# Performance work log

Hardware: AMD Instinct MI355X
Metric: run time of the kernel (lower is better)

Reference implementation:

```python
import jax, jax.numpy as jnp
import numpy as np

EPS = 1e-12


def setup_inputs() -> dict:
    key = jax.random.key(0)
    k1, k2, k3, k4 = jax.random.split(key, 4)
    N, H, W, D, K = 64, 32, 32, 512, 64
    x = jax.random.normal(k1, (N, H, W, D), dtype=jnp.float32)
    W_assign = jax.random.normal(k2, (D, K), dtype=jnp.float32) * 0.05  # 1x1 conv kernel
    b_assign = jax.random.normal(k3, (K,), dtype=jnp.float32) * 0.05
    C = jax.random.normal(k4, (D, K), dtype=jnp.float32) * 0.05  # cluster centers
    return {"x": x, "W_assign": W_assign, "b_assign": b_assign, "C": C}


def _l2norm(v, axis):
    return v / jnp.sqrt(jnp.sum(v * v, axis=axis, keepdims=True) + EPS)


def reference(x, W_assign, b_assign, C):
    # 1x1 conv = matmul over channel dim: [N,H,W,D] @ [D,K] -> [N,H,W,K]
    s = jnp.einsum('nhwd,dk->nhwk', x, W_assign) + b_assign
    a = jax.nn.softmax(s, axis=-1)                       # soft assignment over K
    # VLAD: v[n,d,k] = sum_hw a[n,h,w,k] * (x[n,h,w,d] + C[d,k])
    # reformulated as two small contractions (no [N,H,W,D,K] intermediate):
    v = jnp.einsum('nhwd,nhwk->ndk', x, a)               # feature-weighted sums
    a_sum = jnp.sum(a, axis=(1, 2))                      # [N,K]
    v = v + a_sum[:, None, :] * C[None, :, :]            # [N,D,K]
    # intra-normalization: L2 over D per cluster (after transpose to [N,K,D])
    v = _l2norm(jnp.transpose(v, (0, 2, 1)), axis=-1)    # [N,K,D]
    v = jnp.transpose(v, (0, 2, 1))                      # [N,D,K]
    # flatten and final L2 normalize -> [N, D*K]
    v = v.reshape(v.shape[0], -1)
    return _l2norm(v, axis=-1)
```

## Files before the change

kernel.cpp:

```cpp
#include <hip/hip_runtime.h>


#define EPSF 1e-12f

typedef short bf16x8 __attribute__((ext_vector_type(8)));
typedef float f32x16 __attribute__((ext_vector_type(16)));

__device__ inline unsigned short f2bf_rne(float f) {
  union { float f; unsigned u; } v; v.f = f;
  unsigned u = v.u;
  unsigned r = u + 0x7fffu + ((u >> 16) & 1u);
  return (unsigned short)(r >> 16);
}
__device__ inline unsigned pk2(float a, float b) {
  return (unsigned)f2bf_rne(a) | ((unsigned)f2bf_rne(b) << 16);
}

__global__ __launch_bounds__(256) void kprep(
    const float* __restrict__ Wm, unsigned short* __restrict__ wt) {
  __shared__ float tile[64][65];
  const int t = threadIdx.x, bx = blockIdx.x;
  {
    int col = (t & 15) * 4, rbase = t >> 4;
#pragma unroll
    for (int r = 0; r < 4; ++r) {
      int row = rbase + 16 * r;
      *(float4*)&tile[row][col] =
          *(const float4*)&Wm[(size_t)(bx * 64 + row) * 64 + col];
    }
  }
  __syncthreads();
  int k = t >> 2, seg = (t & 3) * 16;
  size_t o = (size_t)k * 512 + bx * 64 + seg;
#pragma unroll
  for (int j = 0; j < 16; j += 2)
    *(unsigned*)&wt[o + j] = pk2(tile[seg + j][k], tile[seg + j + 1][k]);
}

__global__ __launch_bounds__(256) void kconv(
    const float* __restrict__ x, unsigned short* __restrict__ xt) {
  __shared__ unsigned short td[64][66];
  const int t = threadIdx.x;
  const int hw0 = (blockIdx.x & 15) * 64, d0 = (blockIdx.x >> 4) * 64;
  const int n = blockIdx.y;
  {
    int c = (t & 15) * 4, r0 = t >> 4;
#pragma unroll
    for (int rr = 0; rr < 4; ++rr) {
      int row = r0 + 16 * rr;
      float4 v = *(const float4*)&x[((size_t)(n * 1024 + hw0 + row)) * 512 + d0 + c];
      *(unsigned*)&td[row][c] = pk2(v.x, v.y);
      *(unsigned*)&td[row][c + 2] = pk2(v.z, v.w);
    }
  }
  __syncthreads();
  const int d = t >> 2, hs = (t & 3) * 16;
  unsigned o[8];
#pragma unroll
  for (int j = 0; j < 8; ++j)
    o[j] = (unsigned)td[hs + 2 * j][d] | ((unsigned)td[hs + 2 * j + 1][d] << 16);
  size_t g = ((size_t)n * 512 + d0 + d) * 1024 + hw0 + hs;
  *(uint4*)&xt[g] = *(uint4*)&o[0];
  *(uint4*)&xt[g + 8] = *(uint4*)&o[4];
}

__global__ __launch_bounds__(256) void kassign(
    const float* __restrict__ x, const unsigned short* __restrict__ wt,
    const float* __restrict__ b, unsigned short* __restrict__ at,
    float* __restrict__ a_sum) {
  __shared__ unsigned short xs[128][72];
  __shared__ unsigned short ws[64][72];
  const int t = threadIdx.x;
  const int w = t >> 6, lane = t & 63, l31 = lane & 31, h = lane >> 5;
  const int p0 = blockIdx.x * 128;
  const int col = (t & 15) * 4, rbase = t >> 4;
  const int wk = t >> 2, wseg = (t & 3) * 16;

  float4 px[8];
  uint4 pw0, pw1;
#pragma unroll
  for (int r = 0; r < 8; ++r)
    px[r] = *(const float4*)&x[(size_t)(p0 + rbase + 16 * r) * 512 + col];
  pw0 = *(const uint4*)&wt[(size_t)wk * 512 + wseg];
  pw1 = *(const uint4*)&wt[(size_t)wk * 512 + wseg + 8];

  f32x16 acc0, acc1;
#pragma unroll
  for (int i = 0; i < 16; ++i) { acc0[i] = 0.f; acc1[i] = 0.f; }

  for (int c = 0; c < 8; ++c) {
    __syncthreads();
#pragma unroll
    for (int r = 0; r < 8; ++r) {
      uint2 ph;
      ph.x = pk2(px[r].x, px[r].y);
      ph.y = pk2(px[r].z, px[r].w);
      *(uint2*)&xs[rbase + 16 * r][col] = ph;
    }
    *(uint4*)&ws[wk][wseg] = pw0;
    *(uint4*)&ws[wk][wseg + 8] = pw1;
    __syncthreads();
    if (c < 7) {
      const int dc = (c + 1) * 64;
#pragma unroll
      for (int r = 0; r < 8; ++r)
        px[r] = *(const float4*)&x[(size_t)(p0 + rbase + 16 * r) * 512 + dc + col];
      pw0 = *(const uint4*)&wt[(size_t)wk * 512 + dc + wseg];
      pw1 = *(const uint4*)&wt[(size_t)wk * 512 + dc + wseg + 8];
    }
#pragma unroll
    for (int s = 0; s < 4; ++s) {
      int kd = s * 16 + h * 8;
      bf16x8 ax = *(const bf16x8*)&xs[32 * w + l31][kd];
      bf16x8 b0 = *(const bf16x8*)&ws[l31][kd];
      bf16x8 b1 = *(const bf16x8*)&ws[32 + l31][kd];
      acc0 = __builtin_amdgcn_mfma_f32_32x32x16_bf16(ax, b0, acc0, 0, 0, 0);
      acc1 = __builtin_amdgcn_mfma_f32_32x32x16_bf16(ax, b1, acc1, 0, 0, 0);
    }
  }

  const float bias0 = b[l31], bias1 = b[32 + l31];
  float a0[16], a1[16];
  float sum0 = 0.f, sum1 = 0.f;
#pragma unroll
  for (int r = 0; r < 16; ++r) {
    float s0 = acc0[r] + bias0, s1 = acc1[r] + bias1;
    float m = fmaxf(s0, s1);
#pragma unroll
    for (int msk = 1; msk < 32; msk <<= 1) m = fmaxf(m, __shfl_xor(m, msk, 64));
    float e0 = __expf(s0 - m), e1 = __expf(s1 - m);
    float S = e0 + e1;
#pragma unroll
    for (int msk = 1; msk < 32; msk <<= 1) S += __shfl_xor(S, msk, 64);
    float inv = 1.0f / S;
    a0[r] = e0 * inv; a1[r] = e1 * inv;
    sum0 += a0[r]; sum1 += a1[r];
  }
  const int n = p0 >> 10;
  const int hwb = (p0 & 1023) + 32 * w + 4 * h;
  const size_t kb0 = ((size_t)n * 64 + l31) * 1024;
  const size_t kb1 = ((size_t)n * 64 + 32 + l31) * 1024;
#pragma unroll
  for (int g = 0; g < 4; ++g) {
    int hw = hwb + 8 * g;
    uint2 u;
    u.x = pk2(a0[4 * g + 0], a0[4 * g + 1]);
    u.y = pk2(a0[4 * g + 2], a0[4 * g + 3]);
    *(uint2*)&at[kb0 + hw] = u;
    u.x = pk2(a1[4 * g + 0], a1[4 * g + 1]);
    u.y = pk2(a1[4 * g + 2], a1[4 * g + 3]);
    *(uint2*)&at[kb1 + hw] = u;
  }
  sum0 += __shfl_xor(sum0, 32, 64);
  sum1 += __shfl_xor(sum1, 32, 64);
  if (lane < 32) {
    atomicAdd(&a_sum[n * 64 + l31], sum0);
    atomicAdd(&a_sum[n * 64 + 32 + l31], sum1);
  }
}

__global__ __launch_bounds__(256) void kvlad(
    const unsigned short* __restrict__ xt, const unsigned short* __restrict__ at,
    const float* __restrict__ a_sum, const float* __restrict__ C,
    float* __restrict__ out, float* __restrict__ ssq) {
  __shared__ unsigned short xa[64][72];
  __shared__ unsigned short as_[64][72];
  const int t = threadIdx.x;
  const int w = t >> 6, lane = t & 63, l31 = lane & 31, h = lane >> 5;
  const int n = blockIdx.y, d0 = blockIdx.x * 64;
  const int dw = 32 * (w & 1), kw = 32 * (w >> 1);
  const int sd = t >> 2, sseg = (t & 3) * 16;
  const size_t xbase = ((size_t)n * 512 + d0 + sd) * 1024;
  const size_t abase = ((size_t)n * 64 + sd) * 1024;

  uint4 px0, px1, pa0, pa1;
  px0 = *(const uint4*)&xt[xbase + sseg];
  px1 = *(const uint4*)&xt[xbase + sseg + 8];
  pa0 = *(const uint4*)&at[abase + sseg];
  pa1 = *(const uint4*)&at[abase + sseg + 8];

  f32x16 acc;
#pragma unroll
  for (int i = 0; i < 16; ++i) acc[i] = 0.f;

  for (int c = 0; c < 16; ++c) {
    __syncthreads();
    *(uint4*)&xa[sd][sseg] = px0;
    *(uint4*)&xa[sd][sseg + 8] = px1;
    *(uint4*)&as_[sd][sseg] = pa0;
    *(uint4*)&as_[sd][sseg + 8] = pa1;
    __syncthreads();
    if (c < 15) {
      const int hw0 = (c + 1) * 64;
      px0 = *(const uint4*)&xt[xbase + hw0 + sseg];
      px1 = *(const uint4*)&xt[xbase + hw0 + sseg + 8];
      pa0 = *(const uint4*)&at[abase + hw0 + sseg];
      pa1 = *(const uint4*)&at[abase + hw0 + sseg + 8];
    }
#pragma unroll
    for (int s = 0; s < 4; ++s) {
      int kk = s * 16 + h * 8;
      bf16x8 ax = *(const bf16x8*)&xa[dw + l31][kk];
      bf16x8 bb = *(const bf16x8*)&as_[kw + l31][kk];
      acc = __builtin_amdgcn_mfma_f32_32x32x16_bf16(ax, bb, acc, 0, 0, 0);
    }
  }

  const int k = kw + l31;
  const float as = a_sum[n * 64 + k];
  float sq = 0.f;
#pragma unroll
  for (int r = 0; r < 16; ++r) {
    int row = (r & 3) + 8 * (r >> 2) + 4 * h;
    int d = d0 + dw + row;
    float o = acc[r] + as * C[(size_t)d * 64 + k];
    out[((size_t)n * 512 + d) * 64 + k] = o;
    sq += o * o;
  }
  atomicAdd(&ssq[n * 64 + k], sq);
}

__global__ __launch_bounds__(256) void kscale(
    float* __restrict__ out, const float* __restrict__ ssq) {
  const int n = blockIdx.y, slice = blockIdx.x;
  const int t = threadIdx.x, k = t & 63, rg = t >> 6;
  __shared__ float sk[64];
  __shared__ float tot;
  if (t < 64) {
    float c = ssq[n * 64 + t];
    sk[t] = rsqrtf(c + EPSF);
    float contrib = c / (c + EPSF);
#pragma unroll
    for (int m = 32; m; m >>= 1) contrib += __shfl_xor(contrib, m, 64);
    if (t == 0) tot = rsqrtf(contrib + EPSF);
  }
  __syncthreads();
  const float scale = sk[k] * tot;
  float* vb = out + (size_t)n * 32768 + (size_t)slice * 4096;
#pragma unroll
  for (int r = rg; r < 64; r += 4) vb[r * 64 + k] *= scale;
}

extern "C" void kernel_launch(void* const* d_in, const int* in_sizes, int n_in,
                              void* d_out, int out_size, void* d_ws, size_t ws_size,
                              hipStream_t stream) {
  const float* x  = (const float*)d_in[0];
  const float* Wm = (const float*)d_in[1];
  const float* b  = (const float*)d_in[2];
  const float* C  = (const float*)d_in[3];
  float* out = (float*)d_out;

  unsigned short* at = (unsigned short*)d_ws;
  unsigned short* xt = at + (size_t)64 * 64 * 1024;
  unsigned short* wt = xt + (size_t)64 * 512 * 1024;
  float* a_sum = (float*)(wt + (size_t)64 * 512);
  float* ssq   = a_sum + 4096;

  hipMemsetAsync(a_sum, 0, 8192 * sizeof(float), stream);
  kprep<<<dim3(8), dim3(256), 0, stream>>>(Wm, wt);
  kconv<<<dim3(128, 64), dim3(256), 0, stream>>>(x, xt);
  kassign<<<dim3(512), dim3(256), 0, stream>>>(x, wt, b, at, a_sum);
  kvlad<<<dim3(8, 64), dim3(256), 0, stream>>>(xt, at, a_sum, C, out, ssq);
  kscale<<<dim3(8, 64), dim3(256), 0, stream>>>(out, ssq);
}
```

Measured before the change: 260.4 us.

## Fuse bf16 transpose of x into assignment kernel, drop separate conversion pass

Removes the standalone kconv kernel and has kassign write the transposed bf16 copy of x directly from the registers it already loads for the matmul. The per-thread load pattern changes so each thread holds 8 consecutive pixels, which lets it pack them into 16-byte stores along the hw dimension. This avoids reading x (128 MB of fp32) a second time and saves one kernel launch, at the cost of extra store traffic and register pressure in kassign. It also swaps the software bf16 rounding for the hardware packed-convert builtin when the compiler provides it.

```diff
diff --git a/kernel.cpp b/kernel.cpp
--- a/kernel.cpp
+++ b/kernel.cpp
@@ -13,7 +13,12 @@
   return (unsigned short)(r >> 16);
 }
 __device__ inline unsigned pk2(float a, float b) {
+#if __has_builtin(__builtin_amdgcn_cvt_pk_bf16_f32)
+  auto r = __builtin_amdgcn_cvt_pk_bf16_f32(a, b);
+  return __builtin_bit_cast(unsigned, r);
+#else
   return (unsigned)f2bf_rne(a) | ((unsigned)f2bf_rne(b) << 16);
+#endif
 }
 
 __global__ __launch_bounds__(256) void kprep(
@@ -37,50 +42,25 @@
     *(unsigned*)&wt[o + j] = pk2(tile[seg + j][k], tile[seg + j + 1][k]);
 }
 
-__global__ __launch_bounds__(256) void kconv(
-    const float* __restrict__ x, unsigned short* __restrict__ xt) {
-  __shared__ unsigned short td[64][66];
-  const int t = threadIdx.x;
-  const int hw0 = (blockIdx.x & 15) * 64, d0 = (blockIdx.x >> 4) * 64;
-  const int n = blockIdx.y;
-  {
-    int c = (t & 15) * 4, r0 = t >> 4;
-#pragma unroll
-    for (int rr = 0; rr < 4; ++rr) {
-      int row = r0 + 16 * rr;
-      float4 v = *(const float4*)&x[((size_t)(n * 1024 + hw0 + row)) * 512 + d0 + c];
-      *(unsigned*)&td[row][c] = pk2(v.x, v.y);
-      *(unsigned*)&td[row][c + 2] = pk2(v.z, v.w);
-    }
-  }
-  __syncthreads();
-  const int d = t >> 2, hs = (t & 3) * 16;
-  unsigned o[8];
-#pragma unroll
-  for (int j = 0; j < 8; ++j)
-    o[j] = (unsigned)td[hs + 2 * j][d] | ((unsigned)td[hs + 2 * j + 1][d] << 16);
-  size_t g = ((size_t)n * 512 + d0 + d) * 1024 + hw0 + hs;
-  *(uint4*)&xt[g] = *(uint4*)&o[0];
-  *(uint4*)&xt[g + 8] = *(uint4*)&o[4];
-}
-
 __global__ __launch_bounds__(256) void kassign(
     const float* __restrict__ x, const unsigned short* __restrict__ wt,
     const float* __restrict__ b, unsigned short* __restrict__ at,
-    float* __restrict__ a_sum) {
+    unsigned short* __restrict__ xt, float* __restrict__ a_sum) {
   __shared__ unsigned short xs[128][72];
   __shared__ unsigned short ws[64][72];
   const int t = threadIdx.x;
   const int w = t >> 6, lane = t & 63, l31 = lane & 31, h = lane >> 5;
   const int p0 = blockIdx.x * 128;
-  const int col = (t & 15) * 4, rbase = t >> 4;
+  const int n = p0 >> 10;
+  const int hwbase = p0 & 1023;
+  const int q8 = (t >> 4) * 8, c4 = (t & 15) * 4;
   const int wk = t >> 2, wseg = (t & 3) * 16;
 
   float4 px[8];
   uint4 pw0, pw1;
 #pragma unroll
-  for (int r = 0; r < 8; ++r)
-    px[r] = *(const float4*)&x[(size_t)(p0 + rbase + 16 * r) * 512 + col];
+  for (int j = 0; j < 8; ++j)
+    px[j] = *(const float4*)&x[(size_t)(p0 + q8 + j) * 512 + c4];
   pw0 = *(const uint4*)&wt[(size_t)wk * 512 + wseg];
   pw1 = *(const uint4*)&wt[(size_t)wk * 512 + wseg + 8];
 
@@ -89,24 +69,38 @@
   for (int i = 0; i < 16; ++i) { acc0[i] = 0.f; acc1[i] = 0.f; }
 
   for (int c = 0; c < 8; ++c) {
-    __syncthreads();
-#pragma unroll
-    for (int r = 0; r < 8; ++r) {
+    const int dc = c * 64;
+    __syncthreads();
+#pragma unroll
+    for (int j = 0; j < 8; ++j) {
       uint2 ph;
-      ph.x = pk2(px[r].x, px[r].y);
-      ph.y = pk2(px[r].z, px[r].w);
-      *(uint2*)&xs[rbase + 16 * r][col] = ph;
+      ph.x = pk2(px[j].x, px[j].y);
+      ph.y = pk2(px[j].z, px[j].w);
+      *(uint2*)&xs[q8 + j][c4] = ph;
     }
     *(uint4*)&ws[wk][wseg] = pw0;
     *(uint4*)&ws[wk][wseg + 8] = pw1;
+    {
+      const float* p = (const float*)px;
+#pragma unroll
+      for (int i = 0; i < 4; ++i) {
+        uint4 o;
+        o.x = pk2(px[0][i], px[1][i]);
+        o.y = pk2(px[2][i], px[3][i]);
+        o.z = pk2(px[4][i], px[5][i]);
+        o.w = pk2(px[6][i], px[7][i]);
+        *(uint4*)&xt[((size_t)n * 512 + dc + c4 + i) * 1024 + hwbase + q8] = o;
+      }
+      (void)p;
+    }
     __syncthreads();
     if (c < 7) {
-      const int dc = (c + 1) * 64;
-#pragma unroll
-      for (int r = 0; r < 8; ++r)
-        px[r] = *(const float4*)&x[(size_t)(p0 + rbase + 16 * r) * 512 + dc + col];
-      pw0 = *(const uint4*)&wt[(size_t)wk * 512 + dc + wseg];
-      pw1 = *(const uint4*)&wt[(size_t)wk * 512 + dc + wseg + 8];
+      const int dn = (c + 1) * 64;
+#pragma unroll
+      for (int j = 0; j < 8; ++j)
+        px[j] = *(const float4*)&x[(size_t)(p0 + q8 + j) * 512 + dn + c4];
+      pw0 = *(const uint4*)&wt[(size_t)wk * 512 + dn + wseg];
+      pw1 = *(const uint4*)&wt[(size_t)wk * 512 + dn + wseg + 8];
     }
 #pragma unroll
     for (int s = 0; s < 4; ++s) {
@@ -136,8 +130,7 @@
     a0[r] = e0 * inv; a1[r] = e1 * inv;
     sum0 += a0[r]; sum1 += a1[r];
   }
-  const int n = p0 >> 10;
-  const int hwb = (p0 & 1023) + 32 * w + 4 * h;
+  const int hwb = hwbase + 32 * w + 4 * h;
   const size_t kb0 = ((size_t)n * 64 + l31) * 1024;
   const size_t kb1 = ((size_t)n * 64 + 32 + l31) * 1024;
 #pragma unroll
@@ -258,8 +251,7 @@
 
   hipMemsetAsync(a_sum, 0, 8192 * sizeof(float), stream);
   kprep<<<dim3(8), dim3(256), 0, stream>>>(Wm, wt);
-  kconv<<<dim3(128, 64), dim3(256), 0, stream>>>(x, xt);
-  kassign<<<dim3(512), dim3(256), 0, stream>>>(x, wt, b, at, a_sum);
+  kassign<<<dim3(512), dim3(256), 0, stream>>>(x, wt, b, at, xt, a_sum);
   kvlad<<<dim3(8, 64), dim3(256), 0, stream>>>(xt, at, a_sum, C, out, ssq);
   kscale<<<dim3(8, 64), dim3(256), 0, stream>>>(out, ssq);
 }
```

Measured after the change: 246.3 us. 1.06x faster.
